# Optimization experiments

Hardware: AMD Instinct MI355X
Metric: run time of the kernel (lower is better)

Reference implementation:

```python
import jax, jax.numpy as jnp
import numpy as np

# Equal-capacity grouped-GEMM view of megablocks SparseMLP:
# tokens are pre-sorted by expert; topo's block-sparsity is equivalent to a
# per-expert dense GEMM over that expert's token slice.
E, T, H, F = 8, 2048, 1024, 4096  # experts, tokens/expert, hidden, ffn_hidden


def setup_inputs() -> dict:
    key = jax.random.key(0)
    k1, k2, k3 = jax.random.split(key, 3)
    x = jax.random.normal(k1, (E, T, H), dtype=jnp.float32)
    w1 = jax.random.normal(k2, (E, F, H), dtype=jnp.float32) * 0.02
    w2 = jax.random.normal(k3, (E, F, H), dtype=jnp.float32) * 0.02
    return {"x": x, "w1": w1, "w2": w2}


def reference(x, w1, w2):
    # sdd(x, w1.t(), topo): per-expert x_e @ w1_e^T -> [E, T, F]
    h = jnp.einsum('eth,efh->etf', x, w1)
    # megablocks DEFAULT_ACTIVATION_FN = gelu(approximate='tanh')
    a = jax.nn.gelu(h, approximate=True)
    # dsd(act, w2): per-expert a_e @ w2_e -> [E, T, H]
    return jnp.einsum('etf,efh->eth', a, w2)
```

## Files before the change

kernel.cpp:

```cpp
#include <hip/hip_runtime.h>
#include <hip/hip_bf16.h>


typedef __bf16 bf16x8 __attribute__((ext_vector_type(8)));
typedef float  f32x16 __attribute__((ext_vector_type(16)));

__device__ inline unsigned short f2b(float f) {
    unsigned u = __float_as_uint(f);
    u += 0x7fff + ((u >> 16) & 1);
    return (unsigned short)(u >> 16);
}

__global__ void cast_f32_bf16(const float* __restrict__ in,
                              unsigned short* __restrict__ out, int n4) {
    int i = blockIdx.x * 256 + threadIdx.x;
    if (i >= n4) return;
    float4 v = ((const float4*)in)[i];
    ushort4 o;
    o.x = f2b(v.x); o.y = f2b(v.y); o.z = f2b(v.z); o.w = f2b(v.w);
    ((ushort4*)out)[i] = o;
}

__global__ void transpose_cast(const float* __restrict__ in,
                               unsigned short* __restrict__ out, int F, int H) {
    __shared__ float tile[32][33];
    const int e = blockIdx.z;
    const int f0 = blockIdx.y * 32, h0 = blockIdx.x * 32;
    const float* src = in + (long long)e * F * H;
    unsigned short* dst = out + (long long)e * F * H;
    const int tx = threadIdx.x, ty = threadIdx.y;
#pragma unroll
    for (int i = 0; i < 32; i += 8)
        tile[ty + i][tx] = src[(long long)(f0 + ty + i) * H + h0 + tx];
    __syncthreads();
#pragma unroll
    for (int i = 0; i < 32; i += 8)
        dst[(long long)(h0 + ty + i) * F + f0 + tx] = f2b(tile[tx][ty + i]);
}

template <bool GELU, bool RASTER1D, typename CT>
__global__ __launch_bounds__(256) void gemm_bt(
    const unsigned short* __restrict__ A,
    const unsigned short* __restrict__ B,
    CT* __restrict__ C, int M, int N, int K) {
    int e, bm, bn;
    if constexpr (RASTER1D) {
        const int id = blockIdx.x;
        const int xcd = id & 7, s = id >> 3, t = s & 15;
        e  = s >> 4;
        bm = (xcd * 2 + (t >> 3)) * 128;
        bn = (t & 7) * 128;
    } else {
        e = blockIdx.z; bm = blockIdx.y * 128; bn = blockIdx.x * 128;
    }
    A += (long long)e * M * K;
    B += (long long)e * N * K;
    C += (long long)e * M * N;

    __shared__ unsigned short sA[128 * 64];
    __shared__ unsigned short sB[128 * 64];

    const int tid  = threadIdx.x;
    const int lane = tid & 63;
    const int wave = tid >> 6;
    const int half = lane >> 5, r32 = lane & 31;
    const int wm = (wave & 1) * 64, wn = (wave >> 1) * 64;

    f32x16 acc[2][2] = {};

    for (int k0 = 0; k0 < K; k0 += 64) {
#pragma unroll
        for (int r = 0; r < 4; ++r) {
            const int eoff = r * 2048 + tid * 8;
            const int row = eoff >> 6;
            const int cD  = (eoff >> 3) & 7;
            const int scol = ((cD ^ (row & 7)) << 3);
            const unsigned short* ga = A + (long long)(bm + row) * K + k0 + scol;
            const unsigned short* gb = B + (long long)(bn + row) * K + k0 + scol;
            __builtin_amdgcn_global_load_lds(
                (const __attribute__((address_space(1))) void*)ga,
                (__attribute__((address_space(3))) void*)(&sA[eoff]), 16, 0, 0);
            __builtin_amdgcn_global_load_lds(
                (const __attribute__((address_space(1))) void*)gb,
                (__attribute__((address_space(3))) void*)(&sB[eoff]), 16, 0, 0);
        }
        __syncthreads();

#pragma unroll
        for (int ks = 0; ks < 4; ++ks) {
            bf16x8 af[2], bfr[2];
            const int cL = ks * 2 + half;
#pragma unroll
            for (int i = 0; i < 2; ++i) {
                const int ra = wm + i * 32 + r32;
                const int rb = wn + i * 32 + r32;
                af[i]  = *(const bf16x8*)&sA[ra * 64 + ((cL ^ (ra & 7)) << 3)];
                bfr[i] = *(const bf16x8*)&sB[rb * 64 + ((cL ^ (rb & 7)) << 3)];
            }
#pragma unroll
            for (int i = 0; i < 2; ++i)
#pragma unroll
                for (int j = 0; j < 2; ++j)
                    acc[i][j] = __builtin_amdgcn_mfma_f32_32x32x16_bf16(
                        af[i], bfr[j], acc[i][j], 0, 0, 0);
        }
        __syncthreads();
    }

#pragma unroll
    for (int i = 0; i < 2; ++i) {
        const int row_base = bm + wm + i * 32;
#pragma unroll
        for (int j = 0; j < 2; ++j) {
            const int col = bn + wn + j * 32 + r32;
#pragma unroll
            for (int r = 0; r < 16; ++r) {
                const int row = row_base + (r & 3) + 8 * (r >> 2) + 4 * half;
                float v = acc[i][j][r];
                if (GELU) {
                    float t = 1.5957691216057308f * (v + 0.044715f * v * v * v);
                    v = v / (1.0f + __expf(-t));
                }
                if constexpr (sizeof(CT) == 2) {
                    ((unsigned short*)C)[(long long)row * N + col] = f2b(v);
                } else {
                    ((float*)C)[(long long)row * N + col] = v;
                }
            }
        }
    }
}

extern "C" void kernel_launch(void* const* d_in, const int* in_sizes, int n_in,
                              void* d_out, int out_size, void* d_ws, size_t ws_size,
                              hipStream_t stream) {
    constexpr int E = 8, T = 2048, H = 1024, F = 4096;
    const float* x  = (const float*)d_in[0];
    const float* w1 = (const float*)d_in[1];
    const float* w2 = (const float*)d_in[2];
    float* out = (float*)d_out;

    unsigned short* xb  = (unsigned short*)d_ws;
    unsigned short* w1b = xb  + (size_t)E * T * H;
    unsigned short* w2t = w1b + (size_t)E * F * H;
    unsigned short* ab  = w2t + (size_t)E * F * H;

    const int nx = E * T * H / 4, nw = E * F * H / 4;
    cast_f32_bf16<<<(nx + 255) / 256, 256, 0, stream>>>(x, xb, nx);
    cast_f32_bf16<<<(nw + 255) / 256, 256, 0, stream>>>(w1, w1b, nw);
    transpose_cast<<<dim3(H / 32, F / 32, E), dim3(32, 8), 0, stream>>>(w2, w2t, F, H);

    gemm_bt<true, false, unsigned short>
        <<<dim3(F / 128, T / 128, E), 256, 0, stream>>>(xb, w1b, ab, T, F, H);
    gemm_bt<false, true, float>
        <<<dim3(E * (T / 128) * (H / 128)), 256, 0, stream>>>(ab, w2t, out, T, H, F);
}
```

Before: 678.7 us.

## Rewrite grouped GEMM as 256x256 tile, 8-wave, double-buffered ping-pong pipeline

Replaces the 128x128 single-buffered GEMM with a 256x256 tile kernel using 512 threads, double-buffered LDS, and interleaved prefetch of the next K tiles between MFMA phases with s_setprio and explicit waitcnt control. It also adds an extended LDS swizzle, an XCD-aware 1D block mapping for both GEMMs, and widens the transpose-cast to write ushort2. The aim is to hide global load latency behind MFMA work and raise arithmetic intensity per tile. In exchange it uses much more LDS and registers, so occupancy drops, and the grid for the second GEMM shrinks to 256 blocks.

```diff
diff --git a/kernel.cpp b/kernel.cpp
--- a/kernel.cpp
+++ b/kernel.cpp
@@ -9,6 +9,10 @@
     unsigned u = __float_as_uint(f);
     u += 0x7fff + ((u >> 16) & 1);
     return (unsigned short)(u >> 16);
+}
+
+__device__ inline int swz(int row, int cL) {
+    return (cL ^ (row & 7) ^ (((row >> 3) & 3) << 1)) << 3;
 }
 
 __global__ void cast_f32_bf16(const float* __restrict__ in,
@@ -23,100 +27,184 @@
 
 __global__ void transpose_cast(const float* __restrict__ in,
                                unsigned short* __restrict__ out, int F, int H) {
-    __shared__ float tile[32][33];
+    __shared__ float tile[64][33];
     const int e = blockIdx.z;
-    const int f0 = blockIdx.y * 32, h0 = blockIdx.x * 32;
+    const int f0 = blockIdx.y * 64, h0 = blockIdx.x * 32;
     const float* src = in + (long long)e * F * H;
     unsigned short* dst = out + (long long)e * F * H;
     const int tx = threadIdx.x, ty = threadIdx.y;
 #pragma unroll
-    for (int i = 0; i < 32; i += 8)
+    for (int i = 0; i < 64; i += 8)
         tile[ty + i][tx] = src[(long long)(f0 + ty + i) * H + h0 + tx];
     __syncthreads();
 #pragma unroll
-    for (int i = 0; i < 32; i += 8)
-        dst[(long long)(h0 + ty + i) * F + f0 + tx] = f2b(tile[tx][ty + i]);
-}
-
-template <bool GELU, bool RASTER1D, typename CT>
-__global__ __launch_bounds__(256) void gemm_bt(
+    for (int i = 0; i < 32; i += 8) {
+        const int h = ty + i;
+        ushort2 o;
+        o.x = f2b(tile[2 * tx][h]);
+        o.y = f2b(tile[2 * tx + 1][h]);
+        *(ushort2*)&dst[(long long)(h0 + h) * F + f0 + 2 * tx] = o;
+    }
+}
+
+#define STG(dst, g, q, kt)                                                    \
+    __builtin_amdgcn_global_load_lds(                                         \
+        (const __attribute__((address_space(1))) void*)((g) +                 \
+            (long long)((q) * 64 + srow) * K + ((kt) << 6) + scol),           \
+        (__attribute__((address_space(3))) void*)(&(dst)[(q) * 4096 + sdst]), \
+        16, 0, 0)
+
+template <bool GELU, typename CT>
+__global__ __launch_bounds__(512) void gemm_bt8(
     const unsigned short* __restrict__ A,
     const unsigned short* __restrict__ B,
     CT* __restrict__ C, int M, int N, int K) {
-    int e, bm, bn;
-    if constexpr (RASTER1D) {
-        const int id = blockIdx.x;
-        const int xcd = id & 7, s = id >> 3, t = s & 15;
-        e  = s >> 4;
-        bm = (xcd * 2 + (t >> 3)) * 128;
-        bn = (t & 7) * 128;
-    } else {
-        e = blockIdx.z; bm = blockIdx.y * 128; bn = blockIdx.x * 128;
-    }
+    const int nwg = gridDim.x;
+    const int id = blockIdx.x;
+    const int wgid = (id & 7) * (nwg >> 3) + (id >> 3);
+    const int ntn = N >> 8;
+    const int tpe = (M >> 8) * ntn;
+    const int e = wgid / tpe;
+    const int rem = wgid - e * tpe;
+    const int bm = (rem / ntn) << 8;
+    const int bn = (rem % ntn) << 8;
     A += (long long)e * M * K;
     B += (long long)e * N * K;
     C += (long long)e * M * N;
 
-    __shared__ unsigned short sA[128 * 64];
-    __shared__ unsigned short sB[128 * 64];
-
-    const int tid  = threadIdx.x;
+    __shared__ __align__(16) unsigned short sA[2][256 * 64];
+    __shared__ __align__(16) unsigned short sB[2][256 * 64];
+
+    const int tid = threadIdx.x;
     const int lane = tid & 63;
-    const int wave = tid >> 6;
+    const int wid = tid >> 6;
     const int half = lane >> 5, r32 = lane & 31;
-    const int wm = (wave & 1) * 64, wn = (wave >> 1) * 64;
-
-    f32x16 acc[2][2] = {};
-
-    for (int k0 = 0; k0 < K; k0 += 64) {
-#pragma unroll
-        for (int r = 0; r < 4; ++r) {
-            const int eoff = r * 2048 + tid * 8;
-            const int row = eoff >> 6;
-            const int cD  = (eoff >> 3) & 7;
-            const int scol = ((cD ^ (row & 7)) << 3);
-            const unsigned short* ga = A + (long long)(bm + row) * K + k0 + scol;
-            const unsigned short* gb = B + (long long)(bn + row) * K + k0 + scol;
-            __builtin_amdgcn_global_load_lds(
-                (const __attribute__((address_space(1))) void*)ga,
-                (__attribute__((address_space(3))) void*)(&sA[eoff]), 16, 0, 0);
-            __builtin_amdgcn_global_load_lds(
-                (const __attribute__((address_space(1))) void*)gb,
-                (__attribute__((address_space(3))) void*)(&sB[eoff]), 16, 0, 0);
-        }
-        __syncthreads();
-
-#pragma unroll
-        for (int ks = 0; ks < 4; ++ks) {
-            bf16x8 af[2], bfr[2];
-            const int cL = ks * 2 + half;
-#pragma unroll
-            for (int i = 0; i < 2; ++i) {
-                const int ra = wm + i * 32 + r32;
-                const int rb = wn + i * 32 + r32;
-                af[i]  = *(const bf16x8*)&sA[ra * 64 + ((cL ^ (ra & 7)) << 3)];
-                bfr[i] = *(const bf16x8*)&sB[rb * 64 + ((cL ^ (rb & 7)) << 3)];
-            }
-#pragma unroll
-            for (int i = 0; i < 2; ++i)
-#pragma unroll
-                for (int j = 0; j < 2; ++j)
-                    acc[i][j] = __builtin_amdgcn_mfma_f32_32x32x16_bf16(
-                        af[i], bfr[j], acc[i][j], 0, 0, 0);
-        }
-        __syncthreads();
-    }
-
-#pragma unroll
-    for (int i = 0; i < 2; ++i) {
-        const int row_base = bm + wm + i * 32;
-#pragma unroll
-        for (int j = 0; j < 2; ++j) {
-            const int col = bn + wn + j * 32 + r32;
+    const int wm = (wid >> 2) * 128;
+    const int wn = (wid & 3) * 64;
+
+    const int srow = tid >> 3;
+    const int scol = ((tid & 7) ^ ((tid >> 3) & 7) ^ (((tid >> 6) & 3) << 1)) << 3;
+    const int sdst = tid * 8;
+
+    const unsigned short* gA = A + (long long)bm * K;
+    const unsigned short* gB = B + (long long)bn * K;
+    const int NT = K >> 6;
+
+    {
+        unsigned short* dA = sA[0];
+        unsigned short* dB = sB[0];
+        STG(dB, gB, 0, 0); STG(dB, gB, 1, 0); STG(dB, gB, 2, 0); STG(dB, gB, 3, 0);
+        STG(dA, gA, 0, 0); STG(dA, gA, 2, 0); STG(dA, gA, 1, 0); STG(dA, gA, 3, 0);
+        if (NT > 1) {
+            unsigned short* dB1 = sB[1];
+            STG(dB1, gB, 0, 1); STG(dB1, gB, 1, 1); STG(dB1, gB, 2, 1); STG(dB1, gB, 3, 1);
+            asm volatile("s_waitcnt vmcnt(4)" ::: "memory");
+        } else {
+            asm volatile("s_waitcnt vmcnt(0)" ::: "memory");
+        }
+    }
+    __builtin_amdgcn_s_barrier();
+
+    f32x16 acc[4][2] = {};
+    bf16x8 af[2][4], bf[2][4];
+
+    for (int kt = 0; kt < NT; ++kt) {
+        const int p = kt & 1;
+        const unsigned short* cA = sA[p];
+        const unsigned short* cB = sB[p];
+        unsigned short* nA = sA[p ^ 1];
+        unsigned short* stB = sB[p];
+        const bool pf1 = (kt + 1 < NT), pf2 = (kt + 2 < NT);
+
+#pragma unroll
+        for (int mb = 0; mb < 2; ++mb) {
+            const int row = wm + mb * 32 + r32;
+#pragma unroll
+            for (int ks = 0; ks < 4; ++ks)
+                af[mb][ks] = *(const bf16x8*)&cA[row * 64 + swz(row, ks * 2 + half)];
+        }
+        {
+            const int row = wn + r32;
+#pragma unroll
+            for (int ks = 0; ks < 4; ++ks)
+                bf[0][ks] = *(const bf16x8*)&cB[row * 64 + swz(row, ks * 2 + half)];
+        }
+        if (pf1) { STG(nA, gA, 0, kt + 1); STG(nA, gA, 2, kt + 1); }
+        __builtin_amdgcn_s_barrier();
+        asm volatile("s_waitcnt lgkmcnt(0)" ::: "memory");
+        __builtin_amdgcn_s_setprio(1);
+#pragma unroll
+        for (int ks = 0; ks < 4; ++ks)
+#pragma unroll
+            for (int mb = 0; mb < 2; ++mb)
+                acc[mb][0] = __builtin_amdgcn_mfma_f32_32x32x16_bf16(
+                    af[mb][ks], bf[0][ks], acc[mb][0], 0, 0, 0);
+        __builtin_amdgcn_s_setprio(0);
+        __builtin_amdgcn_s_barrier();
+
+        {
+            const int row = wn + 32 + r32;
+#pragma unroll
+            for (int ks = 0; ks < 4; ++ks)
+                bf[1][ks] = *(const bf16x8*)&cB[row * 64 + swz(row, ks * 2 + half)];
+        }
+        if (pf1) { STG(nA, gA, 1, kt + 1); STG(nA, gA, 3, kt + 1); }
+        __builtin_amdgcn_s_barrier();
+        asm volatile("s_waitcnt lgkmcnt(0)" ::: "memory");
+        __builtin_amdgcn_s_setprio(1);
+#pragma unroll
+        for (int ks = 0; ks < 4; ++ks)
+#pragma unroll
+            for (int mb = 0; mb < 2; ++mb)
+                acc[mb][1] = __builtin_amdgcn_mfma_f32_32x32x16_bf16(
+                    af[mb][ks], bf[1][ks], acc[mb][1], 0, 0, 0);
+        __builtin_amdgcn_s_setprio(0);
+        __builtin_amdgcn_s_barrier();
+
+#pragma unroll
+        for (int mb = 0; mb < 2; ++mb) {
+            const int row = wm + 64 + mb * 32 + r32;
+#pragma unroll
+            for (int ks = 0; ks < 4; ++ks)
+                af[mb][ks] = *(const bf16x8*)&cA[row * 64 + swz(row, ks * 2 + half)];
+        }
+        if (pf2) { STG(stB, gB, 0, kt + 2); STG(stB, gB, 1, kt + 2); }
+        __builtin_amdgcn_s_barrier();
+        asm volatile("s_waitcnt lgkmcnt(0)" ::: "memory");
+        __builtin_amdgcn_s_setprio(1);
+#pragma unroll
+        for (int ks = 0; ks < 4; ++ks)
+#pragma unroll
+            for (int mb = 0; mb < 2; ++mb)
+                acc[2 + mb][0] = __builtin_amdgcn_mfma_f32_32x32x16_bf16(
+                    af[mb][ks], bf[0][ks], acc[2 + mb][0], 0, 0, 0);
+        __builtin_amdgcn_s_setprio(0);
+        __builtin_amdgcn_s_barrier();
+
+        if (pf2) { STG(stB, gB, 2, kt + 2); STG(stB, gB, 3, kt + 2); }
+        __builtin_amdgcn_s_setprio(1);
+#pragma unroll
+        for (int ks = 0; ks < 4; ++ks)
+#pragma unroll
+            for (int mb = 0; mb < 2; ++mb)
+                acc[2 + mb][1] = __builtin_amdgcn_mfma_f32_32x32x16_bf16(
+                    af[mb][ks], bf[1][ks], acc[2 + mb][1], 0, 0, 0);
+        __builtin_amdgcn_s_setprio(0);
+        if (pf2) asm volatile("s_waitcnt vmcnt(4)" ::: "memory");
+        else     asm volatile("s_waitcnt vmcnt(0)" ::: "memory");
+        __builtin_amdgcn_s_barrier();
+    }
+
+#pragma unroll
+    for (int mb = 0; mb < 4; ++mb) {
+        const int row_base = bm + wm + mb * 32;
+#pragma unroll
+        for (int nb = 0; nb < 2; ++nb) {
+            const int col = bn + wn + nb * 32 + r32;
 #pragma unroll
             for (int r = 0; r < 16; ++r) {
                 const int row = row_base + (r & 3) + 8 * (r >> 2) + 4 * half;
-                float v = acc[i][j][r];
+                float v = acc[mb][nb][r];
                 if (GELU) {
                     float t = 1.5957691216057308f * (v + 0.044715f * v * v * v);
                     v = v / (1.0f + __expf(-t));
@@ -130,6 +218,7 @@
         }
     }
 }
+#undef STG
 
 extern "C" void kernel_launch(void* const* d_in, const int* in_sizes, int n_in,
                               void* d_out, int out_size, void* d_ws, size_t ws_size,
@@ -148,10 +237,10 @@
     const int nx = E * T * H / 4, nw = E * F * H / 4;
     cast_f32_bf16<<<(nx + 255) / 256, 256, 0, stream>>>(x, xb, nx);
     cast_f32_bf16<<<(nw + 255) / 256, 256, 0, stream>>>(w1, w1b, nw);
-    transpose_cast<<<dim3(H / 32, F / 32, E), dim3(32, 8), 0, stream>>>(w2, w2t, F, H);
-
-    gemm_bt<true, false, unsigned short>
-        <<<dim3(F / 128, T / 128, E), 256, 0, stream>>>(xb, w1b, ab, T, F, H);
-    gemm_bt<false, true, float>
-        <<<dim3(E * (T / 128) * (H / 128)), 256, 0, stream>>>(ab, w2t, out, T, H, F);
-}
+    transpose_cast<<<dim3(H / 32, F / 64, E), dim3(32, 8), 0, stream>>>(w2, w2t, F, H);
+
+    gemm_bt8<true, unsigned short>
+        <<<dim3(E * (T / 256) * (F / 256)), 512, 0, stream>>>(xb, w1b, ab, T, F, H);
+    gemm_bt8<false, float>
+        <<<dim3(E * (T / 256) * (H / 256)), 512, 0, stream>>>(ab, w2t, out, T, H, F);
+}
```

Measured after the change: 667.2 us. About the same (-1.7%).
